# Kernel optimization log

Hardware: AMD Instinct MI355X
Metric: run time of the kernel (lower is better)

The kernel has to match this reference:

```python
import jax, jax.numpy as jnp
import numpy as np

P = 7            # cfg.PATCH_SIZE_PHOTOMETRIC
BRIGHT = 0.02    # bright_threshold
BIG = 1e9        # masks invalid points out of kNN
K = 5            # neighbors for smoothness/slope


def _smooth_l1(x, y, beta):
    d = jnp.abs(x - y)
    return jnp.where(d < beta, 0.5 * d * d / beta, d - 0.5 * beta)


def _sample_patches(img, kp):
    # img: [B,1,H,W], kp: [B,N,2] (x,y) in pixel coords -> [B,1,N,P,P]
    # matches F.grid_sample(align_corners=True, bilinear, border): with the
    # module's normalization, sampling positions are exactly pixel coords.
    B, _, H, W = img.shape
    N = kp.shape[1]
    half = P // 2
    lin = jnp.linspace(-half, half, P)
    oy, ox = jnp.meshgrid(lin, lin, indexing='ij')  # patch index (i,j): +x=lin[j], +y=lin[i]
    px = jnp.clip(kp[..., 0:1] + ox.ravel(), 0.0, W - 1)  # [B,N,P*P]
    py = jnp.clip(kp[..., 1:2] + oy.ravel(), 0.0, H - 1)
    x0 = jnp.floor(px); y0 = jnp.floor(py)
    fx = px - x0; fy = py - y0
    x0i = jnp.clip(x0.astype(jnp.int32), 0, W - 1)
    x1i = jnp.clip(x0i + 1, 0, W - 1)
    y0i = jnp.clip(y0.astype(jnp.int32), 0, H - 1)
    y1i = jnp.clip(y0i + 1, 0, H - 1)
    im = img[:, 0]  # [B,H,W]
    b = jnp.arange(B)[:, None, None]
    v00 = im[b, y0i, x0i]; v01 = im[b, y0i, x1i]
    v10 = im[b, y1i, x0i]; v11 = im[b, y1i, x1i]
    val = (v00 * (1 - fx) + v01 * fx) * (1 - fy) + (v10 * (1 - fx) + v11 * fx) * fy
    return val.reshape(B, 1, N, P, P)


def _forward(lg, rg, kpl, kpr, scores, Q):
    B, N, _ = kpl.shape
    # ---- epipolar ----
    y_diff = jnp.abs(kpl[..., 1] - kpr[..., 1])
    ws = scores.sum()
    l_epipolar = jnp.where(ws > 1e-4, (y_diff * scores).sum() / jnp.maximum(ws, 1e-12), y_diff.mean())
    # ---- photometric + intensity ----
    pl = _sample_patches(lg, kpl)
    pr = _sample_patches(rg, kpr)
    c = P // 2
    center_l = pl[:, 0, :, c, c]  # [B,N]
    center_r = pr[:, 0, :, c, c]
    is_bright = (center_l > BRIGHT).astype(pl.dtype)
    diff = jnp.abs(pl - pr).mean(axis=(1, 3, 4))  # [B,N]
    w = scores * is_bright
    wsum = w.sum()
    safe = jnp.maximum(wsum, 1e-12)
    l_masked = jnp.where(wsum > 1e-4, (diff * w).sum() / safe, 0.0)
    l_intensity = jnp.where(wsum > 1e-4, (_smooth_l1(center_l, center_r, 1.0) * w).sum() / safe, 0.0)
    l_photo = l_masked + l_intensity
    # ---- disparity -> 3D ----
    disp = kpl[..., 0] - kpr[..., 0]
    pts4 = jnp.concatenate([kpl, disp[..., None], jnp.ones((B, N, 1), kpl.dtype)], axis=-1)
    proj = jnp.einsum('bni,bji->bnj', pts4, Q)
    Wc = jnp.maximum(proj[..., 3], 1e-6)
    p3d = proj[..., :3] / Wc[..., None]  # [B,N,3]
    Z = p3d[..., 2]
    valid = (Z > 100) & (Z < 30000) & (scores > 0.1)  # [B,N]
    # ---- kNN smoothness / slope / zero-mean (masked, vectorized) ----
    pm = p3d / 1000.0
    xy = pm[..., jnp.array([0, 2])]  # [B,N,2] horizontal plane
    h = pm[..., 1]                   # [B,N] height
    sq = (xy * xy).sum(-1)
    d2 = sq[:, :, None] + sq[:, None, :] - 2.0 * jnp.einsum('bnd,bmd->bnm', xy, xy)
    dist = jnp.sqrt(jnp.maximum(d2, 1e-12))  # [B,N,N]
    vm = valid[:, :, None] & valid[:, None, :]
    dist = jnp.where(vm, dist, BIG)
    negd, idx = jax.lax.top_k(-dist, K + 1)   # ascending distance
    nbr_idx = idx[:, :, 1:]                   # drop self
    nbr_d = jnp.maximum(-negd[:, :, 1:], 1e-3)
    b = jnp.arange(B)[:, None, None]
    nbr_h = h[b, nbr_idx]                     # [B,N,K]
    local_mean = nbr_h.mean(-1)
    n_valid = valid.sum(-1)
    nv = jnp.maximum(n_valid, 1).astype(h.dtype)
    vf = valid.astype(h.dtype)
    ls_b = (_smooth_l1(h, local_mean, 0.01) * vf).sum(-1) / nv
    slopes = jnp.abs(nbr_h - h[..., None]) / nbr_d
    pen = jax.nn.relu(slopes - 0.4)
    lsl_b = (pen * vf[..., None]).sum((-1, -2)) / (nv * K)
    lz_b = jnp.abs((h * vf).sum(-1) / nv)
    ok = (n_valid >= 10).astype(h.dtype)
    nb = jnp.maximum(ok.sum(), 1.0)
    gate = ((scores > 0.1).sum() >= 10) & (ok.sum() > 0)
    l_smooth = jnp.where(gate, (ls_b * ok).sum() / nb, 0.0)
    l_slope = jnp.where(gate, (lsl_b * ok).sum() / nb, 0.0)
    l_zeromean = jnp.where(gate, (lz_b * ok).sum() / nb, 0.0)
    return (l_photo, l_epipolar, l_smooth, l_slope, l_zeromean)


def setup_inputs() -> dict:
    key = jax.random.key(0)
    k = jax.random.split(key, 7)
    B, N, H, W = 16, 2000, 720, 1280
    lg = jax.random.uniform(k[0], (B, 1, H, W), dtype=jnp.float32)
    rg = jax.random.uniform(k[1], (B, 1, H, W), dtype=jnp.float32)
    kx = jax.random.uniform(k[2], (B, N), minval=200.0, maxval=1080.0)
    ky = jax.random.uniform(k[3], (B, N), minval=50.0, maxval=670.0)
    disp = jax.random.uniform(k[4], (B, N), minval=10.0, maxval=200.0)
    kpl = jnp.stack([kx, ky], -1)
    kpr = jnp.stack([kx - disp, ky + 0.5 * jax.random.normal(k[5], (B, N))], -1)
    scores = jax.random.uniform(k[6], (B, N), dtype=jnp.float32)
    f, cx, cy, Tx = 1000.0, 640.0, 360.0, 120.0  # focal px, principal point, baseline mm
    Qm = jnp.array([[1.0, 0.0, 0.0, -cx],
                    [0.0, 1.0, 0.0, -cy],
                    [0.0, 0.0, 0.0, f],
                    [0.0, 0.0, 1.0 / Tx, 0.0]], dtype=jnp.float32)
    Q = jnp.broadcast_to(Qm, (B, 4, 4))
    return {"lg": lg, "rg": rg, "kpl": kpl, "kpr": kpr, "scores": scores, "Q": Q}


def reference(lg, rg, kpl, kpr, scores, Q):
    return _forward(lg, rg, kpl, kpr, scores, Q)
```

## Files before the change

### kernel.cpp

```cpp
#include <hip/hip_runtime.h>

#define BB 16
#define NN 2000
#define HH 720
#define WW 1280
#define NPT (BB*NN)
#define PT_BLOCKS (NPT/32)
#define PPT 4
#define NCHUNK 16
#define NSPLIT 5
#define MSEG (NN/NSPLIT)
#define CK2 (MSEG/NCHUNK)
#define KSTRIDE 2048

static __device__ __forceinline__ unsigned u_min(unsigned a, unsigned b){ return a < b ? a : b; }

static __device__ __forceinline__ unsigned u_med3(unsigned a, unsigned b, unsigned c) {
    unsigned d;
    asm("v_med3_u32 %0, %1, %2, %3" : "=v"(d) : "v"(a), "v"(b), "v"(c));
    return d;
}

__device__ __forceinline__ void ins5(unsigned K[5], unsigned u) {
    K[4] = u_med3(K[3], K[4], u);
    K[3] = u_med3(K[2], K[3], u);
    K[2] = u_med3(K[1], K[2], u);
    K[1] = u_med3(K[0], K[1], u);
    K[0] = u_min(K[0], u);
}

__device__ __forceinline__ float bilin(const float* __restrict__ im, float px, float py) {
    px = fminf(fmaxf(px, 0.f), (float)(WW - 1));
    py = fminf(fmaxf(py, 0.f), (float)(HH - 1));
    float x0f = floorf(px), y0f = floorf(py);
    float fx = px - x0f, fy = py - y0f;
    int x0 = min(max((int)x0f, 0), WW - 1);
    int x1 = min(x0 + 1, WW - 1);
    int y0 = min(max((int)y0f, 0), HH - 1);
    int y1 = min(y0 + 1, HH - 1);
    const float* r0 = im + (size_t)y0 * WW;
    const float* r1 = im + (size_t)y1 * WW;
    float v00 = r0[x0], v01 = r0[x1], v10 = r1[x0], v11 = r1[x1];
    return (v00 * (1.f - fx) + v01 * fx) * (1.f - fy)
         + (v10 * (1.f - fx) + v11 * fx) * fy;
}

__global__ __launch_bounds__(256) void point_kernel(
    const float* __restrict__ lg, const float* __restrict__ rg,
    const float* __restrict__ kpl, const float* __restrict__ kpr,
    const float* __restrict__ scores, const float* __restrict__ Q,
    float4* __restrict__ pts, float* __restrict__ partials,
    float* __restrict__ batch_acc)
{
    if (blockIdx.x == 0 && threadIdx.x < BB * 4) batch_acc[threadIdx.x] = 0.f;

    int wave = threadIdx.x >> 6, lane = threadIdx.x & 63;
    int rr = lane / 7, ci = lane - rr * 7;
    int s00 = lane + rr;
    if (s00 > 54) s00 = 54;
    int reg_r = lane >> 3, reg_c = lane & 7;

    float a0=0.f,a1=0.f,a2=0.f,a3=0.f,a4=0.f,a5=0.f,a6=0.f;

    for (int it = 0; it < 8; ++it) {
        int pt = blockIdx.x * 32 + wave * 8 + it;
        int b = pt / NN;
        const float* iml = lg + (size_t)b * (HH * WW);
        const float* imr = rg + (size_t)b * (HH * WW);
        float kxl = kpl[2*pt], kyl = kpl[2*pt+1];
        float kxr = kpr[2*pt], kyr = kpr[2*pt+1];
        float sc  = scores[pt];

        float flx = floorf(kxl), fly = floorf(kyl);
        int xbl = (int)flx - 3, ybl = (int)fly - 3;
        float fxl = kxl - flx, fyl = kyl - fly;
        float vl = 0.f;
        if (xbl >= 0 && xbl <= WW-8 && ybl >= 0 && ybl <= HH-8) {
            float reg = iml[(size_t)(ybl + reg_r) * WW + xbl + reg_c];
            float v00 = __shfl(reg, s00,     64);
            float v01 = __shfl(reg, s00 + 1, 64);
            float v10 = __shfl(reg, s00 + 8, 64);
            float v11 = __shfl(reg, s00 + 9, 64);
            vl = (v00*(1.f-fxl) + v01*fxl)*(1.f-fyl) + (v10*(1.f-fxl) + v11*fxl)*fyl;
        } else if (lane < 49) {
            vl = bilin(iml, kxl + (float)(ci-3), kyl + (float)(rr-3));
        }
        float frx = floorf(kxr), fry = floorf(kyr);
        int xbr = (int)frx - 3, ybr = (int)fry - 3;
        float fxr = kxr - frx, fyr = kyr - fry;
        float vr = 0.f;
        if (xbr >= 0 && xbr <= WW-8 && ybr >= 0 && ybr <= HH-8) {
            float reg = imr[(size_t)(ybr + reg_r) * WW + xbr + reg_c];
            float v00 = __shfl(reg, s00,     64);
            float v01 = __shfl(reg, s00 + 1, 64);
            float v10 = __shfl(reg, s00 + 8, 64);
            float v11 = __shfl(reg, s00 + 9, 64);
            vr = (v00*(1.f-fxr) + v01*fxr)*(1.f-fyr) + (v10*(1.f-fxr) + v11*fxr)*fyr;
        } else if (lane < 49) {
            vr = bilin(imr, kxr + (float)(ci-3), kyr + (float)(rr-3));
        }

        float adiff = (lane < 49) ? fabsf(vl - vr) : 0.f;
        float cl = __shfl(vl, 24, 64);
        float cr = __shfl(vr, 24, 64);
        #pragma unroll
        for (int off = 32; off > 0; off >>= 1) adiff += __shfl_down(adiff, off, 64);

        if (lane == 0) {
            float diff = adiff / 49.f;
            float isb  = (cl > 0.02f) ? 1.f : 0.f;
            float w    = sc * isb;
            float ydiff = fabsf(kyl - kyr);
            float dc = fabsf(cl - cr);
            float sl1 = (dc < 1.f) ? 0.5f * dc * dc : dc - 0.5f;

            const float* q = Q + b * 16;
            float dsp = kxl - kxr;
            float p0 = q[0]*kxl + q[1]*kyl + q[2]*dsp  + q[3];
            float p1 = q[4]*kxl + q[5]*kyl + q[6]*dsp  + q[7];
            float p2 = q[8]*kxl + q[9]*kyl + q[10]*dsp + q[11];
            float p3 = q[12]*kxl + q[13]*kyl + q[14]*dsp + q[15];
            float Wc = fmaxf(p3, 1e-6f);
            float X = p0 / Wc, Y = p1 / Wc, Z = p2 / Wc;
            bool valid = (Z > 100.f) && (Z < 30000.f) && (sc > 0.1f);
            float x  = X / 1000.f;
            float hh = Y / 1000.f;
            float y  = Z / 1000.f;
            float sq = x * x + y * y;
            if (!valid) { x = 0.f; y = 0.f; sq = 1e18f; }
            pts[pt] = make_float4(x, y, sq, hh);

            a0 += sc;  a1 += ydiff * sc;  a2 += ydiff;
            a3 += w;   a4 += diff * w;    a5 += sl1 * w;
            a6 += (sc > 0.1f) ? 1.f : 0.f;
        }
    }

    __shared__ float red[4][7];
    if (lane == 0) {
        red[wave][0]=a0; red[wave][1]=a1; red[wave][2]=a2; red[wave][3]=a3;
        red[wave][4]=a4; red[wave][5]=a5; red[wave][6]=a6;
    }
    __syncthreads();
    if (threadIdx.x < 8) {
        int k = threadIdx.x;
        float v = 0.f;
        if (k < 7) v = red[0][k] + red[1][k] + red[2][k] + red[3][k];
        partials[blockIdx.x * 8 + k] = v;
    }
}

__global__ __launch_bounds__(256) void knn_scan(
    const float4* __restrict__ pts, unsigned* __restrict__ keybuf)
{
    __shared__ float4 tile[MSEG];
    int b = blockIdx.z, seg = blockIdx.y;
    int mseg0 = seg * MSEG;
    for (int i = threadIdx.x; i < MSEG; i += 256) tile[i] = pts[b * NN + mseg0 + i];
    __syncthreads();

    int lane = threadIdx.x & 63, wave = threadIdx.x >> 6;
    int qi = lane >> 4;
    int c  = lane & 15;
    int n0 = blockIdx.x * 64 + (wave * 4 + qi) * PPT;

    unsigned K[PPT][5];
    float nx2[PPT], ny2[PPT], sqn[PPT];
    #pragma unroll
    for (int j = 0; j < PPT; ++j) {
        int n = n0 + j;
        float4 me = (n < NN) ? pts[b * NN + n] : make_float4(0.f, 0.f, 1e18f, 0.f);
        nx2[j] = -2.f * me.x; ny2[j] = -2.f * me.y; sqn[j] = me.z;
        #pragma unroll
        for (int t = 0; t < 5; ++t) K[j][t] = 0xFFFFFFFFu;
    }

    const int mb = c * CK2;
    bool self_here = (blockIdx.x * 64 + 63 >= mseg0) && (blockIdx.x * 64 < mseg0 + MSEG);

    if (self_here) {
        #pragma unroll 5
        for (int mm = 0; mm < CK2; ++mm) {
            int ml = mb + mm, m = mseg0 + ml;
            float4 o = tile[ml];
            #pragma unroll
            for (int j = 0; j < PPT; ++j) {
                float t = fmaf(ny2[j], o.y, o.z);
                t = fmaf(nx2[j], o.x, t);
                float d2 = fmaxf(t + sqn[j], 1e-12f);
                unsigned u = (__float_as_uint(d2) & 0xFFFFF800u) | (unsigned)m;
                u = (m == n0 + j) ? 0xFFFFFFFFu : u;
                ins5(K[j], u);
            }
        }
    } else {
        #pragma unroll 5
        for (int mm = 0; mm < CK2; ++mm) {
            int ml = mb + mm, m = mseg0 + ml;
            float4 o = tile[ml];
            #pragma unroll
            for (int j = 0; j < PPT; ++j) {
                float t = fmaf(ny2[j], o.y, o.z);
                t = fmaf(nx2[j], o.x, t);
                float d2 = fmaxf(t + sqn[j], 1e-12f);
                unsigned u = (__float_as_uint(d2) & 0xFFFFF800u) | (unsigned)m;
                ins5(K[j], u);
            }
        }
    }

    #pragma unroll
    for (int off = 1; off < 16; off <<= 1) {
        #pragma unroll
        for (int j = 0; j < PPT; ++j) {
            unsigned B0 = (unsigned)__shfl_xor((int)K[j][0], off, 64);
            unsigned B1 = (unsigned)__shfl_xor((int)K[j][1], off, 64);
            unsigned B2 = (unsigned)__shfl_xor((int)K[j][2], off, 64);
            unsigned B3 = (unsigned)__shfl_xor((int)K[j][3], off, 64);
            unsigned B4 = (unsigned)__shfl_xor((int)K[j][4], off, 64);
            ins5(K[j], B0); ins5(K[j], B1); ins5(K[j], B2); ins5(K[j], B3); ins5(K[j], B4);
        }
    }

    if (c < 5) {
        unsigned w0, w1, w2, w3;
        w0 = K[0][0]; w1 = K[1][0]; w2 = K[2][0]; w3 = K[3][0];
        if (c == 1) { w0 = K[0][1]; w1 = K[1][1]; w2 = K[2][1]; w3 = K[3][1]; }
        if (c == 2) { w0 = K[0][2]; w1 = K[1][2]; w2 = K[2][2]; w3 = K[3][2]; }
        if (c == 3) { w0 = K[0][3]; w1 = K[1][3]; w2 = K[2][3]; w3 = K[3][3]; }
        if (c == 4) { w0 = K[0][4]; w1 = K[1][4]; w2 = K[2][4]; w3 = K[3][4]; }
        uint4* dst = (uint4*)&keybuf[(size_t)(((b * NSPLIT + seg) * 5 + c)) * KSTRIDE + n0];
        *dst = make_uint4(w0, w1, w2, w3);
    }
}

__global__ __launch_bounds__(256) void knn_merge(
    const float4* __restrict__ pts, const unsigned* __restrict__ keybuf,
    float* __restrict__ batch_acc)
{
    int b = blockIdx.y;
    int n = blockIdx.x * 256 + threadIdx.x;

    float ls = 0.f, pen = 0.f, hacc = 0.f, cnt = 0.f;
    if (n < NN) {
        float4 me = pts[b * NN + n];
        if (me.z < 1e17f) {
            unsigned K[5] = {0xFFFFFFFFu,0xFFFFFFFFu,0xFFFFFFFFu,0xFFFFFFFFu,0xFFFFFFFFu};
            #pragma unroll
            for (int s = 0; s < NSPLIT; ++s) {
                #pragma unroll
                for (int j = 0; j < 5; ++j) {
                    unsigned u = keybuf[(size_t)((b * NSPLIT + s) * 5 + j) * KSTRIDE + n];
                    ins5(K, u);
                }
            }
            float hsum = 0.f;
            #pragma unroll
            for (int t = 0; t < 5; ++t) {
                int idx = (int)(K[t] & 2047u);
                float4 o = pts[b * NN + idx];
                float dot = me.x * o.x + me.y * o.y;
                float d2 = (me.z + o.z) - 2.f * dot;
                float nd = fmaxf(sqrtf(fmaxf(d2, 1e-12f)), 0.001f);
                hsum += o.w;
                pen  += fmaxf(fabsf(o.w - me.w) / nd - 0.4f, 0.f);
            }
            float lm = hsum / 5.f;
            float dd = fabsf(me.w - lm);
            ls = (dd < 0.01f) ? 0.5f * dd * dd / 0.01f : dd - 0.005f;
            hacc = me.w;
            cnt  = 1.f;
        }
    }

    #pragma unroll
    for (int off = 32; off > 0; off >>= 1) {
        ls   += __shfl_down(ls,   off, 64);
        pen  += __shfl_down(pen,  off, 64);
        hacc += __shfl_down(hacc, off, 64);
        cnt  += __shfl_down(cnt,  off, 64);
    }
    __shared__ float r2[4][4];
    int wave = threadIdx.x >> 6, lane = threadIdx.x & 63;
    if (lane == 0) { r2[wave][0]=cnt; r2[wave][1]=ls; r2[wave][2]=pen; r2[wave][3]=hacc; }
    __syncthreads();
    if (threadIdx.x == 0) {
        float tc = r2[0][0]+r2[1][0]+r2[2][0]+r2[3][0];
        float tl = r2[0][1]+r2[1][1]+r2[2][1]+r2[3][1];
        float tp = r2[0][2]+r2[1][2]+r2[2][2]+r2[3][2];
        float th = r2[0][3]+r2[1][3]+r2[2][3]+r2[3][3];
        atomicAdd(&batch_acc[b * 4 + 0], tc);
        atomicAdd(&batch_acc[b * 4 + 1], tl);
        atomicAdd(&batch_acc[b * 4 + 2], tp);
        atomicAdd(&batch_acc[b * 4 + 3], th);
    }
}

__global__ __launch_bounds__(256) void final_kernel(
    const float* __restrict__ partials, const float* __restrict__ batch_acc,
    float* __restrict__ out)
{
    float s[8] = {0,0,0,0,0,0,0,0};
    for (int r = threadIdx.x; r < PT_BLOCKS; r += 256) {
        #pragma unroll
        for (int k = 0; k < 8; ++k) s[k] += partials[r * 8 + k];
    }
    #pragma unroll
    for (int off = 32; off > 0; off >>= 1) {
        #pragma unroll
        for (int k = 0; k < 8; ++k) s[k] += __shfl_down(s[k], off, 64);
    }
    __shared__ float wsum_s[4][8];
    int wv = threadIdx.x >> 6, lane = threadIdx.x & 63;
    if (lane == 0) {
        #pragma unroll
        for (int k = 0; k < 8; ++k) wsum_s[wv][k] = s[k];
    }
    __syncthreads();
    if (threadIdx.x == 0) {
        float t[8];
        #pragma unroll
        for (int k = 0; k < 8; ++k)
            t[k] = wsum_s[0][k] + wsum_s[1][k] + wsum_s[2][k] + wsum_s[3][k];
        float ssc = t[0], yds = t[1], yd = t[2], wsum = t[3], dw = t[4], iw = t[5], cnts = t[6];

        float l_epi = (ssc > 1e-4f) ? yds / fmaxf(ssc, 1e-12f) : yd / (float)NPT;
        float safe = fmaxf(wsum, 1e-12f);
        float l_photo = (wsum > 1e-4f) ? (dw / safe + iw / safe) : 0.f;

        float als = 0.f, alsl = 0.f, alz = 0.f, okc = 0.f;
        for (int b = 0; b < BB; ++b) {
            float nvf  = batch_acc[b * 4 + 0];
            float lsb  = batch_acc[b * 4 + 1];
            float penb = batch_acc[b * 4 + 2];
            float hb   = batch_acc[b * 4 + 3];
            float nv = fmaxf(nvf, 1.f);
            float ok = (nvf >= 10.f) ? 1.f : 0.f;
            als  += ok * (lsb / nv);
            alsl += ok * (penb / (nv * 5.f));
            alz  += ok * fabsf(hb / nv);
            okc  += ok;
        }
        float nb = fmaxf(okc, 1.f);
        bool gate = (cnts >= 10.f) && (okc > 0.f);
        out[0] = l_photo;
        out[1] = l_epi;
        out[2] = gate ? als / nb : 0.f;
        out[3] = gate ? alsl / nb : 0.f;
        out[4] = gate ? alz / nb : 0.f;
    }
}

extern "C" void kernel_launch(void* const* d_in, const int* in_sizes, int n_in,
                              void* d_out, int out_size, void* d_ws, size_t ws_size,
                              hipStream_t stream)
{
    const float* lg     = (const float*)d_in[0];
    const float* rg     = (const float*)d_in[1];
    const float* kpl    = (const float*)d_in[2];
    const float* kpr    = (const float*)d_in[3];
    const float* scores = (const float*)d_in[4];
    const float* Q      = (const float*)d_in[5];
    float* out = (float*)d_out;

    char* ws = (char*)d_ws;
    float4*   pts       = (float4*)ws;
    float*    partials  = (float*)(ws + 512000);
    float*    batch_acc = (float*)(ws + 544000);
    unsigned* keybuf    = (unsigned*)(ws + 544256);

    point_kernel<<<PT_BLOCKS, 256, 0, stream>>>(lg, rg, kpl, kpr, scores, Q,
                                                pts, partials, batch_acc);
    knn_scan<<<dim3(32, NSPLIT, BB), 256, 0, stream>>>(pts, keybuf);
    knn_merge<<<dim3(8, BB), 256, 0, stream>>>(pts, keybuf, batch_acc);
    final_kernel<<<1, 256, 0, stream>>>(partials, batch_acc, out);
}
```

Baseline: 204.9 us.

## Restructure kNN scan to one query per thread with more candidate splits

The kNN scan kernel now gives each thread a single query point. It reads its candidate segment straight from global memory with block-uniform addresses, replacing the shared-memory tile, the four-queries-per-thread layout and the cross-lane shuffle merge of partial top-5 lists. The candidate set is split into a runtime-chosen number of segments (16 by default, falling back to 8 or 4 when the workspace is small), and the merge kernel loops over that count. This removes the shuffle reduction and LDS staging, but the merge must now fold more partial lists per point and the key buffer grows.

```diff
diff --git a/kernel.cpp b/kernel.cpp
--- a/kernel.cpp
+++ b/kernel.cpp
@@ -6,11 +6,6 @@
 #define WW 1280
 #define NPT (BB*NN)
 #define PT_BLOCKS (NPT/32)
-#define PPT 4
-#define NCHUNK 16
-#define NSPLIT 5
-#define MSEG (NN/NSPLIT)
-#define CK2 (MSEG/NCHUNK)
 #define KSTRIDE 2048
 
 static __device__ __forceinline__ unsigned u_min(unsigned a, unsigned b){ return a < b ? a : b; }
@@ -151,92 +146,61 @@
 }
 
 __global__ __launch_bounds__(256) void knn_scan(
-    const float4* __restrict__ pts, unsigned* __restrict__ keybuf)
-{
-    __shared__ float4 tile[MSEG];
+    const float4* __restrict__ pts, unsigned* __restrict__ keybuf,
+    int msegLen, int ns)
+{
     int b = blockIdx.z, seg = blockIdx.y;
-    int mseg0 = seg * MSEG;
-    for (int i = threadIdx.x; i < MSEG; i += 256) tile[i] = pts[b * NN + mseg0 + i];
-    __syncthreads();
-
-    int lane = threadIdx.x & 63, wave = threadIdx.x >> 6;
-    int qi = lane >> 4;
-    int c  = lane & 15;
-    int n0 = blockIdx.x * 64 + (wave * 4 + qi) * PPT;
-
-    unsigned K[PPT][5];
-    float nx2[PPT], ny2[PPT], sqn[PPT];
-    #pragma unroll
-    for (int j = 0; j < PPT; ++j) {
-        int n = n0 + j;
-        float4 me = (n < NN) ? pts[b * NN + n] : make_float4(0.f, 0.f, 1e18f, 0.f);
-        nx2[j] = -2.f * me.x; ny2[j] = -2.f * me.y; sqn[j] = me.z;
-        #pragma unroll
-        for (int t = 0; t < 5; ++t) K[j][t] = 0xFFFFFFFFu;
-    }
-
-    const int mb = c * CK2;
-    bool self_here = (blockIdx.x * 64 + 63 >= mseg0) && (blockIdx.x * 64 < mseg0 + MSEG);
-
-    if (self_here) {
+    int mseg0 = seg * msegLen;
+    int n = blockIdx.x * 256 + threadIdx.x;
+    int nc = (n < NN) ? n : (NN - 1);
+
+    float4 me = pts[b * NN + nc];
+    float nx2 = -2.f * me.x, ny2 = -2.f * me.y, sqn = me.z;
+
+    unsigned K[5] = {0xFFFFFFFFu,0xFFFFFFFFu,0xFFFFFFFFu,0xFFFFFFFFu,0xFFFFFFFFu};
+
+    const float4* cand = pts + b * NN + mseg0;
+    int nb0 = blockIdx.x * 256;
+    bool has_self = (mseg0 < nb0 + 256) && (mseg0 + msegLen > nb0);
+
+    if (has_self) {
         #pragma unroll 5
-        for (int mm = 0; mm < CK2; ++mm) {
-            int ml = mb + mm, m = mseg0 + ml;
-            float4 o = tile[ml];
-            #pragma unroll
-            for (int j = 0; j < PPT; ++j) {
-                float t = fmaf(ny2[j], o.y, o.z);
-                t = fmaf(nx2[j], o.x, t);
-                float d2 = fmaxf(t + sqn[j], 1e-12f);
-                unsigned u = (__float_as_uint(d2) & 0xFFFFF800u) | (unsigned)m;
-                u = (m == n0 + j) ? 0xFFFFFFFFu : u;
-                ins5(K[j], u);
-            }
+        for (int mm = 0; mm < msegLen; ++mm) {
+            float4 o = cand[mm];
+            int m = mseg0 + mm;
+            float t = fmaf(ny2, o.y, o.z);
+            t = fmaf(nx2, o.x, t);
+            float d2 = fmaxf(t + sqn, 1e-12f);
+            unsigned u = (__float_as_uint(d2) & 0xFFFFF800u) | (unsigned)m;
+            u = (m == n) ? 0xFFFFFFFFu : u;
+            ins5(K, u);
         }
     } else {
         #pragma unroll 5
-        for (int mm = 0; mm < CK2; ++mm) {
-            int ml = mb + mm, m = mseg0 + ml;
-            float4 o = tile[ml];
-            #pragma unroll
-            for (int j = 0; j < PPT; ++j) {
-                float t = fmaf(ny2[j], o.y, o.z);
-                t = fmaf(nx2[j], o.x, t);
-                float d2 = fmaxf(t + sqn[j], 1e-12f);
-                unsigned u = (__float_as_uint(d2) & 0xFFFFF800u) | (unsigned)m;
-                ins5(K[j], u);
-            }
-        }
-    }
-
-    #pragma unroll
-    for (int off = 1; off < 16; off <<= 1) {
-        #pragma unroll
-        for (int j = 0; j < PPT; ++j) {
-            unsigned B0 = (unsigned)__shfl_xor((int)K[j][0], off, 64);
-            unsigned B1 = (unsigned)__shfl_xor((int)K[j][1], off, 64);
-            unsigned B2 = (unsigned)__shfl_xor((int)K[j][2], off, 64);
-            unsigned B3 = (unsigned)__shfl_xor((int)K[j][3], off, 64);
-            unsigned B4 = (unsigned)__shfl_xor((int)K[j][4], off, 64);
-            ins5(K[j], B0); ins5(K[j], B1); ins5(K[j], B2); ins5(K[j], B3); ins5(K[j], B4);
-        }
-    }
-
-    if (c < 5) {
-        unsigned w0, w1, w2, w3;
-        w0 = K[0][0]; w1 = K[1][0]; w2 = K[2][0]; w3 = K[3][0];
-        if (c == 1) { w0 = K[0][1]; w1 = K[1][1]; w2 = K[2][1]; w3 = K[3][1]; }
-        if (c == 2) { w0 = K[0][2]; w1 = K[1][2]; w2 = K[2][2]; w3 = K[3][2]; }
-        if (c == 3) { w0 = K[0][3]; w1 = K[1][3]; w2 = K[2][3]; w3 = K[3][3]; }
-        if (c == 4) { w0 = K[0][4]; w1 = K[1][4]; w2 = K[2][4]; w3 = K[3][4]; }
-        uint4* dst = (uint4*)&keybuf[(size_t)(((b * NSPLIT + seg) * 5 + c)) * KSTRIDE + n0];
-        *dst = make_uint4(w0, w1, w2, w3);
+        for (int mm = 0; mm < msegLen; ++mm) {
+            float4 o = cand[mm];
+            int m = mseg0 + mm;
+            float t = fmaf(ny2, o.y, o.z);
+            t = fmaf(nx2, o.x, t);
+            float d2 = fmaxf(t + sqn, 1e-12f);
+            unsigned u = (__float_as_uint(d2) & 0xFFFFF800u) | (unsigned)m;
+            ins5(K, u);
+        }
+    }
+
+    if (n < NN) {
+        size_t base = (size_t)((b * ns + seg) * 5) * KSTRIDE + n;
+        keybuf[base              ] = K[0];
+        keybuf[base + KSTRIDE    ] = K[1];
+        keybuf[base + KSTRIDE * 2] = K[2];
+        keybuf[base + KSTRIDE * 3] = K[3];
+        keybuf[base + KSTRIDE * 4] = K[4];
     }
 }
 
 __global__ __launch_bounds__(256) void knn_merge(
     const float4* __restrict__ pts, const unsigned* __restrict__ keybuf,
-    float* __restrict__ batch_acc)
+    float* __restrict__ batch_acc, int ns)
 {
     int b = blockIdx.y;
     int n = blockIdx.x * 256 + threadIdx.x;
@@ -246,11 +210,10 @@
         float4 me = pts[b * NN + n];
         if (me.z < 1e17f) {
             unsigned K[5] = {0xFFFFFFFFu,0xFFFFFFFFu,0xFFFFFFFFu,0xFFFFFFFFu,0xFFFFFFFFu};
-            #pragma unroll
-            for (int s = 0; s < NSPLIT; ++s) {
+            for (int s = 0; s < ns; ++s) {
                 #pragma unroll
                 for (int j = 0; j < 5; ++j) {
-                    unsigned u = keybuf[(size_t)((b * NSPLIT + s) * 5 + j) * KSTRIDE + n];
+                    unsigned u = keybuf[(size_t)((b * ns + s) * 5 + j) * KSTRIDE + n];
                     ins5(K, u);
                 }
             }
@@ -369,9 +332,15 @@
     float*    batch_acc = (float*)(ws + 544000);
     unsigned* keybuf    = (unsigned*)(ws + 544256);
 
+    int ns = 16;
+    size_t need = 544256 + (size_t)BB * 16 * 5 * KSTRIDE * 4;
+    if (ws_size < need) ns = 8;
+    if (ws_size < 544256 + (size_t)BB * 8 * 5 * KSTRIDE * 4) ns = 4;
+    int msegLen = NN / ns;
+
     point_kernel<<<PT_BLOCKS, 256, 0, stream>>>(lg, rg, kpl, kpr, scores, Q,
                                                 pts, partials, batch_acc);
-    knn_scan<<<dim3(32, NSPLIT, BB), 256, 0, stream>>>(pts, keybuf);
-    knn_merge<<<dim3(8, BB), 256, 0, stream>>>(pts, keybuf, batch_acc);
+    knn_scan<<<dim3(8, ns, BB), 256, 0, stream>>>(pts, keybuf, msegLen, ns);
+    knn_merge<<<dim3(8, BB), 256, 0, stream>>>(pts, keybuf, batch_acc, ns);
     final_kernel<<<1, 256, 0, stream>>>(partials, batch_acc, out);
 }
```

Result: faster. 190.5 us (-7.0%).
